# Performance work log

Hardware: AMD Instinct MI355X
Metric: run time of the kernel (lower is better)

## Reference

```python
import jax, jax.numpy as jnp
import numpy as np

NB_HEAD = 16
SIZE_PER_HEAD = 64
D_MODEL = NB_HEAD * SIZE_PER_HEAD  # 1024
B, L = 2, 2048
NEG_BIG = 1e12


def setup_inputs() -> dict:
    key = jax.random.key(0)
    ks = jax.random.split(key, 8)
    return {
        "Q_seq": jax.random.normal(ks[0], (B, L, D_MODEL), dtype=jnp.float32),
        "K_seq": jax.random.normal(ks[1], (B, L, D_MODEL), dtype=jnp.float32),
        "V_seq": jax.random.normal(ks[2], (B, L, D_MODEL), dtype=jnp.float32),
        "q_len": jax.random.randint(ks[3], (B, 1), 1, L, dtype=jnp.int32),
        "v_len": jax.random.randint(ks[4], (B, 1), 1, L, dtype=jnp.int32),
        "WQ": jax.random.normal(ks[5], (D_MODEL, D_MODEL), dtype=jnp.float32) * 0.02,
        "WK": jax.random.normal(ks[6], (D_MODEL, D_MODEL), dtype=jnp.float32) * 0.02,
        "WV": jax.random.normal(ks[7], (D_MODEL, D_MODEL), dtype=jnp.float32) * 0.02,
    }


def _len_mask(lens, length, dtype):
    # Keras code: mask = 1 - cumsum(one_hot(len, L)) -> 1 for pos < len, 0 otherwise
    return (jnp.arange(length)[None, :] < lens).astype(dtype)  # [B, L]


def reference(Q_seq, K_seq, V_seq, q_len, v_len, WQ, WK, WV):
    Bq, Lq, _ = Q_seq.shape
    Lk = K_seq.shape[1]
    # QKV projections, split heads: [B, H, L, D]
    q = (Q_seq @ WQ).reshape(Bq, Lq, NB_HEAD, SIZE_PER_HEAD).transpose(0, 2, 1, 3)
    k = (K_seq @ WK).reshape(Bq, Lk, NB_HEAD, SIZE_PER_HEAD).transpose(0, 2, 1, 3)
    v = (V_seq @ WV).reshape(Bq, Lk, NB_HEAD, SIZE_PER_HEAD).transpose(0, 2, 1, 3)
    # scaled dot-product scores [B, H, Lq, Lk]
    scores = jnp.einsum("bhqd,bhkd->bhqk", q, k) / np.float32(SIZE_PER_HEAD ** 0.5)
    # additive key-length mask (V_len), matching Mask(..., 'add')
    kmask = _len_mask(v_len, Lk, scores.dtype)  # [B, Lk]
    scores = scores - (1.0 - kmask)[:, None, None, :] * np.float32(NEG_BIG)
    A = jax.nn.softmax(scores, axis=-1)
    # attention output, merge heads: [B, Lq, H*D]
    O = jnp.einsum("bhqk,bhkd->bqhd", A, v).reshape(Bq, Lq, D_MODEL)
    # multiplicative query-length mask (Q_len), matching Mask(..., 'mul')
    qmask = _len_mask(q_len, Lq, O.dtype)  # [B, Lq]
    return O * qmask[:, :, None]
```

## Files before the change

kernel.cpp:

```cpp
#include <hip/hip_runtime.h>
#include <cstddef>

#define NB_HEAD 16
#define HEAD_DIM 64
#define D_MODEL 1024
#define BATCH 2
#define SEQ 2048
#define MROWS (BATCH * SEQ)
#define NSPLIT 3

typedef __bf16 bf16x8 __attribute__((ext_vector_type(8)));
typedef __bf16 bf16x4 __attribute__((ext_vector_type(4)));
typedef __bf16 bf16x2 __attribute__((ext_vector_type(2)));
typedef float  f32x4  __attribute__((ext_vector_type(4)));

#define XEL ((size_t)MROWS * D_MODEL)
#define WEL ((size_t)D_MODEL * D_MODEL)

#define QSCALE 0.18033688011112042f

static __device__ __forceinline__ size_t xchunk(int row, int k) {
    return ((size_t)(row >> 4) * 32 + (k >> 5)) * 512 + ((k >> 3) & 3) * 128 + (row & 15) * 8 + (k & 7);
}
static __device__ __forceinline__ size_t qkbase(int bh, int row16, int dc) {
    return ((size_t)(bh * 128 + row16) * 2 + dc) * 512;
}
static __device__ __forceinline__ size_t qkelem(int bh, int row, int d) {
    return qkbase(bh, row >> 4, d >> 5) + ((d >> 3) & 3) * 128 + (row & 15) * 8 + (d & 7);
}
static __device__ __forceinline__ size_t vbase(int bh, int d16, int kc) {
    return ((size_t)(bh * 4 + d16) * 64 + kc) * 512;
}
static __device__ __forceinline__ size_t velem(int bh, int d, int key) {
    return vbase(bh, d >> 4, key >> 5) + ((key >> 3) & 3) * 128 + (d & 15) * 8 + (key & 7);
}

static __device__ __forceinline__ void split_bf16(float x, __bf16& h, __bf16& l) {
    h = (__bf16)x;
    l = (__bf16)(x - (float)h);
}

static __device__ __forceinline__ void gload_lds16(const __bf16* g, __bf16* l) {
    __builtin_amdgcn_global_load_lds((const __attribute__((address_space(1))) void*)g,
                                     (__attribute__((address_space(3))) void*)l,
                                     16, 0, 0);
}

__global__ __launch_bounds__(256) void conv_wt_kernel(
    const float* __restrict__ W0, const float* __restrict__ W1,
    const float* __restrict__ W2,
    __bf16* __restrict__ hi, __bf16* __restrict__ lo)
{
    __shared__ float tile[64][65];
    const int t  = threadIdx.x;
    const int k0 = blockIdx.x * 64;
    const int n0 = blockIdx.y * 64;
    const int z  = blockIdx.z;
    const float* W = (z == 0) ? W0 : ((z == 1) ? W1 : W2);
    __bf16* hz = hi + (size_t)z * WEL;
    __bf16* lz = lo + (size_t)z * WEL;

    #pragma unroll
    for (int p = 0; p < 4; ++p) {
        const int e = (p * 256 + t) * 4;
        const int r = e >> 6, c = e & 63;
        const float4 v = *(const float4*)(W + (size_t)(k0 + r) * D_MODEL + n0 + c);
        tile[r][c] = v.x; tile[r][c + 1] = v.y; tile[r][c + 2] = v.z; tile[r][c + 3] = v.w;
    }
    __syncthreads();
    #pragma unroll
    for (int p = 0; p < 4; ++p) {
        const int e = (p * 256 + t) * 4;
        const int n = e >> 6, kc = e & 63;
        __bf16 h[4], l[4];
        #pragma unroll
        for (int u = 0; u < 4; ++u) split_bf16(tile[kc + u][n], h[u], l[u]);
        const size_t a = xchunk(n0 + n, k0 + kc);
        *(bf16x4*)(hz + a) = (bf16x4){h[0], h[1], h[2], h[3]};
        *(bf16x4*)(lz + a) = (bf16x4){l[0], l[1], l[2], l[3]};
    }
}

__global__ __launch_bounds__(256) void conv_x_kernel(
    const float* __restrict__ X0, const float* __restrict__ X1,
    const float* __restrict__ X2,
    const int* __restrict__ q_len, const int* __restrict__ v_len,
    __bf16* __restrict__ xhi, __bf16* __restrict__ xlo)
{
    const int z = blockIdx.y;
    const size_t e = ((size_t)blockIdx.x * 256 + threadIdx.x) * 8;
    const int l = (int)(e >> 10), k = (int)(e & 1023);
    const int bb = l >> 11, lb = l & (SEQ - 1);
    const int len = (z == 0) ? q_len[bb] : v_len[bb];
    if (lb >= ((len + 127) & ~127)) return;

    const float* X = (z == 0) ? X0 : ((z == 1) ? X1 : X2);
    const float4 v0 = *(const float4*)(X + e);
    const float4 v1 = *(const float4*)(X + e + 4);
    const float xs[8] = {v0.x, v0.y, v0.z, v0.w, v1.x, v1.y, v1.z, v1.w};
    bf16x8 h8, l8;
    #pragma unroll
    for (int u = 0; u < 8; ++u) { __bf16 h_, l_; split_bf16(xs[u], h_, l_); h8[u] = h_; l8[u] = l_; }
    const size_t a = z * XEL + xchunk(l, k);
    *(bf16x8*)(xhi + a) = h8;
    *(bf16x8*)(xlo + a) = l8;
}

__global__ __launch_bounds__(256, 3) void proj_mfma_kernel(
    const __bf16* __restrict__ Xhi, const __bf16* __restrict__ Xlo,
    const __bf16* __restrict__ Wchi, const __bf16* __restrict__ Wclo,
    const int* __restrict__ q_len, const int* __restrict__ v_len,
    __bf16* __restrict__ qch, __bf16* __restrict__ qcl,
    __bf16* __restrict__ kch, __bf16* __restrict__ kcl,
    __bf16* __restrict__ vch, __bf16* __restrict__ vcl)
{
    __shared__ __align__(16) __bf16 lds[2][16][512];

    const int t    = threadIdx.x;
    const int wave = t >> 6, lane = t & 63;
    const int li   = lane & 15, grp = lane >> 4;
    const int wm   = wave >> 1, wn = wave & 1;
    const int m0   = blockIdx.x * 128;
    const int n0   = blockIdx.y * 64;
    const int z    = blockIdx.z;
    const int bb   = m0 >> 11;
    const int l0   = m0 & (SEQ - 1);
    const int need = (z == 0) ? q_len[bb] : v_len[bb];
    if (l0 >= need) return;

    const __bf16* Xh = Xhi + z * XEL;
    const __bf16* Xl = Xlo + z * XEL;
    const __bf16* Wh = Wchi + z * WEL;
    const __bf16* Wl = Wclo + z * WEL;

    const __bf16* gsA[4];
    #pragma unroll
    for (int u = 0; u < 4; ++u) {
        const int c = u * 4 + wave;
        const __bf16* src = (c < 8) ? Xh : Xl;
        const int idx = (m0 >> 4) + (c & 7);
        gsA[u] = src + (size_t)idx * 32 * 512 + (size_t)lane * 8;
    }

    const __bf16* gBh[2];
    const __bf16* gBl[2];
    #pragma unroll
    for (int j = 0; j < 2; ++j) {
        const int idx = (n0 >> 4) + wn * 2 + j;
        gBh[j] = Wh + (size_t)idx * 32 * 512 + (size_t)lane * 8;
        gBl[j] = Wl + (size_t)idx * 32 * 512 + (size_t)lane * 8;
    }

    auto STAGE = [&](int buf, int kc) {
        #pragma unroll
        for (int u = 0; u < 4; ++u)
            gload_lds16(gsA[u] + (size_t)kc * 512, &lds[buf][u * 4 + wave][0]);
    };

    f32x4 acc[4][2] = {};
    bf16x8 bhc[2], blc[2], bhn[2], bln[2];

    STAGE(0, 0);
    #pragma unroll
    for (int j = 0; j < 2; ++j) {
        bhc[j] = *(const bf16x8*)(gBh[j]);
        blc[j] = *(const bf16x8*)(gBl[j]);
    }
    __syncthreads();

    #pragma unroll 2
    for (int kc = 0; kc < 32; ++kc) {
        const int cur = kc & 1;
        if (kc < 31) {
            STAGE(cur ^ 1, kc + 1);
            #pragma unroll
            for (int j = 0; j < 2; ++j) {
                bhn[j] = *(const bf16x8*)(gBh[j] + (size_t)(kc + 1) * 512);
                bln[j] = *(const bf16x8*)(gBl[j] + (size_t)(kc + 1) * 512);
            }
        }

        bf16x8 ah[4], al4[4];
        #pragma unroll
        for (int i = 0; i < 4; ++i) {
            ah[i]  = *(const bf16x8*)&lds[cur][(wm << 2) + i][lane * 8];
            al4[i] = *(const bf16x8*)&lds[cur][8 + (wm << 2) + i][lane * 8];
        }
        #pragma unroll
        for (int j = 0; j < 2; ++j) {
            #pragma unroll
            for (int i = 0; i < 4; ++i) {
                acc[i][j] = __builtin_amdgcn_mfma_f32_16x16x32_bf16(ah[i],  bhc[j], acc[i][j], 0, 0, 0);
                acc[i][j] = __builtin_amdgcn_mfma_f32_16x16x32_bf16(ah[i],  blc[j], acc[i][j], 0, 0, 0);
                acc[i][j] = __builtin_amdgcn_mfma_f32_16x16x32_bf16(al4[i], bhc[j], acc[i][j], 0, 0, 0);
            }
        }
        __syncthreads();
        #pragma unroll
        for (int j = 0; j < 2; ++j) { bhc[j] = bhn[j]; blc[j] = bln[j]; }
    }

    #pragma unroll
    for (int j = 0; j < 2; ++j) {
        const int cg = n0 + wn * 32 + j * 16 + li;
        const int hd = cg >> 6, d = cg & 63;
        const int bhI = bb * NB_HEAD + hd;
        #pragma unroll
        for (int i = 0; i < 4; ++i) {
            #pragma unroll
            for (int r = 0; r < 4; ++r) {
                const int rg = m0 + wm * 64 + i * 16 + grp * 4 + r;
                const int lg = rg & (SEQ - 1);
                __bf16 h_, l_;
                if (z == 0) {
                    split_bf16(acc[i][j][r] * QSCALE, h_, l_);
                    const size_t a = qkelem(bhI, lg, d);
                    qch[a] = h_; qcl[a] = l_;
                } else if (z == 1) {
                    split_bf16(acc[i][j][r], h_, l_);
                    const size_t a = qkelem(bhI, lg, d);
                    kch[a] = h_; kcl[a] = l_;
                } else {
                    split_bf16(acc[i][j][r], h_, l_);
                    const size_t a = velem(bhI, d, lg);
                    vch[a] = h_; vcl[a] = l_;
                }
            }
        }
    }
}

__global__ __launch_bounds__(256, 2) void attn_mfma_kernel(
    const __bf16* __restrict__ qch, const __bf16* __restrict__ qcl,
    const __bf16* __restrict__ kch, const __bf16* __restrict__ kcl,
    const __bf16* __restrict__ vch, const __bf16* __restrict__ vcl,
    const int* __restrict__ q_len, const int* __restrict__ v_len,
    float* __restrict__ Opart, float* __restrict__ Mbuf, float* __restrict__ Lbuf)
{
    __shared__ __align__(16) __bf16 Ps[128][72];

    const int t = threadIdx.x;
    const int wq = t >> 6, lane = t & 63;
    const int grp = lane >> 4, li = lane & 15;
    const int hh = blockIdx.x;
    const int split = (int)(blockIdx.y % NSPLIT);
    const int q0 = (int)(blockIdx.y / NSPLIT) * 128;
    const int b  = blockIdx.z;
    const int qlen = q_len[b], vlen = v_len[b];
    const int bh = b * NB_HEAD + hh;
    const int qbase = q0 + wq * 32;

    if (qbase >= qlen) return;

    bf16x8 onesv;
    #pragma unroll
    for (int u = 0; u < 8; ++u) onesv[u] = (__bf16)1.0f;

    bf16x8 qh[2][2], ql[2][2];
    #pragma unroll
    for (int s = 0; s < 2; ++s)
        #pragma unroll
        for (int ks = 0; ks < 2; ++ks) {
            const size_t a = qkbase(bh, (qbase >> 4) + s, ks) + lane * 8;
            qh[s][ks] = *(const bf16x8*)(qch + a);
            ql[s][ks] = *(const bf16x8*)(qcl + a);
        }

    f32x4 O[2][4] = {};
    float m_s[2] = {-1e30f, -1e30f};
    float l_s[2][4];
    #pragma unroll
    for (int s = 0; s < 2; ++s)
        #pragma unroll
        for (int r = 0; r < 4; ++r) l_s[s][r] = 0.f;

    const int nktT = (vlen + 63) >> 6;
    const int part = (nktT + NSPLIT - 1) / NSPLIT;
    const int tBeg = split * part;
    const int tEnd = (nktT < tBeg + part) ? nktT : (tBeg + part);

    for (int tt = tBeg; tt < tEnd; ++tt) {
        const int k0 = tt * 64;
        const bool full = (k0 + 64 <= vlen);

        f32x4 sacc[2][4] = {};
        #pragma unroll
        for (int ks = 0; ks < 2; ++ks) {
            bf16x8 kh_[4], kl_[4];
            #pragma unroll
            for (int j = 0; j < 4; ++j) {
                const size_t a = qkbase(bh, (k0 >> 4) + j, ks) + lane * 8;
                kh_[j] = *(const bf16x8*)(kch + a);
                kl_[j] = *(const bf16x8*)(kcl + a);
            }
            __builtin_amdgcn_s_setprio(1);
            #pragma unroll
            for (int j = 0; j < 4; ++j)
                #pragma unroll
                for (int s = 0; s < 2; ++s) {
                    sacc[s][j] = __builtin_amdgcn_mfma_f32_16x16x32_bf16(kh_[j], qh[s][ks], sacc[s][j], 0, 0, 0);
                    sacc[s][j] = __builtin_amdgcn_mfma_f32_16x16x32_bf16(kl_[j], qh[s][ks], sacc[s][j], 0, 0, 0);
                    sacc[s][j] = __builtin_amdgcn_mfma_f32_16x16x32_bf16(kh_[j], ql[s][ks], sacc[s][j], 0, 0, 0);
                }
            __builtin_amdgcn_s_setprio(0);
        }

        bf16x8 vh_[2][4], vl_[2][4];
        #pragma unroll
        for (int ks = 0; ks < 2; ++ks)
            #pragma unroll
            for (int j = 0; j < 4; ++j) {
                const size_t a = vbase(bh, j, (k0 >> 5) + ks) + lane * 8;
                vh_[ks][j] = *(const bf16x8*)(vch + a);
                vl_[ks][j] = *(const bf16x8*)(vcl + a);
            }

        float mx[2];
        int defer = 1;
        #pragma unroll
        for (int s = 0; s < 2; ++s) {
            if (!full) {
                #pragma unroll
                for (int j = 0; j < 4; ++j) {
                    const int keyb = k0 + j * 16 + grp * 4;
                    #pragma unroll
                    for (int r = 0; r < 4; ++r)
                        if (keyb + r >= vlen) sacc[s][j][r] = -1e30f;
                }
            }
            float m0_ = -1e30f;
            #pragma unroll
            for (int j = 0; j < 4; ++j)
                #pragma unroll
                for (int r = 0; r < 4; ++r) m0_ = fmaxf(m0_, sacc[s][j][r]);
            m0_ = fmaxf(m0_, __shfl_xor(m0_, 16));
            m0_ = fmaxf(m0_, __shfl_xor(m0_, 32));
            mx[s] = m0_;
            defer &= (m0_ - m_s[s] <= 8.f) ? 1 : 0;
        }

        if (!__all(defer)) {
            #pragma unroll
            for (int s = 0; s < 2; ++s) {
                const float mn = fmaxf(m_s[s], mx[s]);
                const float alq = exp2f(m_s[s] - mn);
                m_s[s] = mn;
                #pragma unroll
                for (int r = 0; r < 4; ++r) {
                    const float alr = __shfl(alq, grp * 4 + r);
                    l_s[s][r] *= alr;
                    #pragma unroll
                    for (int j = 0; j < 4; ++j) O[s][j][r] *= alr;
                }
            }
        }

        #pragma unroll
        for (int s = 0; s < 2; ++s) {
            const int row = wq * 32 + s * 16 + li;
            #pragma unroll
            for (int j = 0; j < 4; ++j) {
                const int col = j * 16 + grp * 4;
                bf16x2 w01, w23;
                w01[0] = (__bf16)exp2f(sacc[s][j][0] - m_s[s]);
                w01[1] = (__bf16)exp2f(sacc[s][j][1] - m_s[s]);
                w23[0] = (__bf16)exp2f(sacc[s][j][2] - m_s[s]);
                w23[1] = (__bf16)exp2f(sacc[s][j][3] - m_s[s]);
                *(bf16x2*)&Ps[row][col]     = w01;
                *(bf16x2*)&Ps[row][col + 2] = w23;
            }
        }
        asm volatile("s_waitcnt lgkmcnt(0)" ::: "memory");

        bf16x8 pa[2][2];
        #pragma unroll
        for (int s = 0; s < 2; ++s)
            #pragma unroll
            for (int ks = 0; ks < 2; ++ks)
                pa[s][ks] = *(const bf16x8*)&Ps[wq * 32 + s * 16 + li][ks * 32 + grp * 8];

        __builtin_amdgcn_s_setprio(1);
        #pragma unroll
        for (int s = 0; s < 2; ++s) {
            f32x4 lsum = {};
            lsum = __builtin_amdgcn_mfma_f32_16x16x32_bf16(pa[s][0], onesv, lsum, 0, 0, 0);
            lsum = __builtin_amdgcn_mfma_f32_16x16x32_bf16(pa[s][1], onesv, lsum, 0, 0, 0);
            #pragma unroll
            for (int r = 0; r < 4; ++r) l_s[s][r] += lsum[r];
        }

        #pragma unroll
        for (int ks = 0; ks < 2; ++ks)
            #pragma unroll
            for (int j = 0; j < 4; ++j)
                #pragma unroll
                for (int s = 0; s < 2; ++s) {
                    O[s][j] = __builtin_amdgcn_mfma_f32_16x16x32_bf16(pa[s][ks], vh_[ks][j], O[s][j], 0, 0, 0);
                    O[s][j] = __builtin_amdgcn_mfma_f32_16x16x32_bf16(pa[s][ks], vl_[ks][j], O[s][j], 0, 0, 0);
                }
        __builtin_amdgcn_s_setprio(0);
    }

    const size_t osplit = (size_t)split * MROWS * D_MODEL;
    #pragma unroll
    for (int s = 0; s < 2; ++s)
        #pragma unroll
        for (int r = 0; r < 4; ++r) {
            const int q = qbase + s * 16 + grp * 4 + r;
            if (q < qlen) {
                #pragma unroll
                for (int j = 0; j < 4; ++j)
                    Opart[osplit + ((size_t)b * SEQ + q) * D_MODEL + hh * HEAD_DIM + j * 16 + li] = O[s][j][r];
                if (li == 0) {
                    const size_t mi = (((size_t)split * BATCH + b) * NB_HEAD + hh) * SEQ + q;
                    Lbuf[mi] = l_s[s][r];
                }
            }
        }
    #pragma unroll
    for (int s = 0; s < 2; ++s) {
        const int q = qbase + s * 16 + li;
        if (grp == 0 && q < qlen) {
            const size_t mi = (((size_t)split * BATCH + b) * NB_HEAD + hh) * SEQ + q;
            Mbuf[mi] = m_s[s];
        }
    }
}

__global__ __launch_bounds__(256) void attn_merge_kernel(
    const float* __restrict__ Opart, const float* __restrict__ Mbuf,
    const float* __restrict__ Lbuf, const int* __restrict__ q_len,
    float* __restrict__ out)
{
    const int row = blockIdx.x;
    const int b = row >> 11, q = row & (SEQ - 1);
    const int col = threadIdx.x * 4;
    const int hh = col >> 6;
    const size_t oidx = (size_t)row * D_MODEL + col;

    float4 o = make_float4(0.f, 0.f, 0.f, 0.f);
    if (q < q_len[b]) {
        const size_t mlsz = (size_t)BATCH * NB_HEAD * SEQ;
        const size_t mi = ((size_t)b * NB_HEAD + hh) * SEQ + q;
        float ms[NSPLIT], ls[NSPLIT];
        float M = -1e30f;
        #pragma unroll
        for (int s = 0; s < NSPLIT; ++s) {
            ms[s] = Mbuf[s * mlsz + mi];
            ls[s] = Lbuf[s * mlsz + mi];
            M = fmaxf(M, ms[s]);
        }
        float denom = 0.f;
        float w[NSPLIT];
        #pragma unroll
        for (int s = 0; s < NSPLIT; ++s) {
            w[s] = exp2f(ms[s] - M);
            denom += ls[s] * w[s];
        }
        const float inv = 1.f / denom;
        float acc[4] = {0.f, 0.f, 0.f, 0.f};
        #pragma unroll
        for (int s = 0; s < NSPLIT; ++s) {
            const float4 a = *(const float4*)(Opart + (size_t)s * MROWS * D_MODEL + oidx);
            acc[0] += a.x * w[s]; acc[1] += a.y * w[s];
            acc[2] += a.z * w[s]; acc[3] += a.w * w[s];
        }
        o.x = acc[0] * inv; o.y = acc[1] * inv; o.z = acc[2] * inv; o.w = acc[3] * inv;
    }
    *(float4*)(out + oidx) = o;
}

extern "C" void kernel_launch(void* const* d_in, const int* in_sizes, int n_in,
                              void* d_out, int out_size, void* d_ws, size_t ws_size,
                              hipStream_t stream)
{
    (void)in_sizes; (void)n_in; (void)out_size; (void)ws_size;
    const float* Q_seq = (const float*)d_in[0];
    const float* K_seq = (const float*)d_in[1];
    const float* V_seq = (const float*)d_in[2];
    const int*   q_len = (const int*)d_in[3];
    const int*   v_len = (const int*)d_in[4];
    const float* WQ    = (const float*)d_in[5];
    const float* WK    = (const float*)d_in[6];
    const float* WV    = (const float*)d_in[7];
    float* out = (float*)d_out;

    __bf16* wchi = (__bf16*)d_ws;
    __bf16* wclo = wchi + 3 * WEL;
    __bf16* xhi_ = wclo + 3 * WEL;
    __bf16* xlo_ = xhi_ + 3 * XEL;
    __bf16* qch_ = xlo_ + 3 * XEL;
    __bf16* qcl_ = qch_ + XEL;
    __bf16* kch_ = qcl_ + XEL;
    __bf16* kcl_ = kch_ + XEL;
    __bf16* vch_ = kcl_ + XEL;
    __bf16* vcl_ = vch_ + XEL;

    float* Opart = (float*)xhi_;
    float* Mbuf  = (float*)wchi;
    float* Lbuf  = Mbuf + (size_t)NSPLIT * BATCH * NB_HEAD * SEQ;

    dim3 blk(256);

    dim3 cg(D_MODEL / 64, D_MODEL / 64, 3);
    conv_wt_kernel<<<cg, blk, 0, stream>>>(WQ, WK, WV, wchi, wclo);

    dim3 xg((unsigned)(XEL / 2048), 3);
    conv_x_kernel<<<xg, blk, 0, stream>>>(Q_seq, K_seq, V_seq, q_len, v_len, xhi_, xlo_);

    dim3 pg(MROWS / 128, D_MODEL / 64, 3);
    proj_mfma_kernel<<<pg, blk, 0, stream>>>(xhi_, xlo_, wchi, wclo, q_len, v_len,
                                             qch_, qcl_, kch_, kcl_, vch_, vcl_);

    dim3 ag(NB_HEAD, (SEQ / 128) * NSPLIT, BATCH);
    attn_mfma_kernel<<<ag, blk, 0, stream>>>(qch_, qcl_, kch_, kcl_, vch_, vcl_,
                                             q_len, v_len, Opart, Mbuf, Lbuf);

    attn_merge_kernel<<<dim3(MROWS), blk, 0, stream>>>(Opart, Mbuf, Lbuf, q_len, out);
}
```

Measured before the change: 255.7 us.

## Triple-buffer projection GEMM with two-stage prefetch and partial vmcnt waits

Converts the projection kernel's double-buffered K loop into a three-stage pipeline. A tiles go to LDS and B fragments go to registers, both loaded two iterations ahead. Full __syncthreads is replaced by explicit s_waitcnt vmcnt(8) plus s_barrier, so in-flight loads for the next stage overlap the MFMAs. The loop is fully unrolled with sched_barriers to pin the order, at the cost of more LDS (48KB vs 32KB) and more VGPRs, which may reduce occupancy below the 3 blocks per CU launch bound.

Measured after the change: 268.2 us. 4.9% more time.

```diff
diff --git a/kernel.cpp b/kernel.cpp
--- a/kernel.cpp
+++ b/kernel.cpp
@@ -114,7 +114,7 @@
     __bf16* __restrict__ kch, __bf16* __restrict__ kcl,
     __bf16* __restrict__ vch, __bf16* __restrict__ vcl)
 {
-    __shared__ __align__(16) __bf16 lds[2][16][512];
+    __shared__ __align__(16) __bf16 lds[3][16][512];
 
     const int t    = threadIdx.x;
     const int wave = t >> 6, lane = t & 63;
@@ -151,34 +151,37 @@
         gBl[j] = Wl + (size_t)idx * 32 * 512 + (size_t)lane * 8;
     }
 
-    auto STAGE = [&](int buf, int kc) {
+    bf16x8 bH[3][2], bL[3][2];
+
+    auto STAGE_A = [&](int buf, int kc) {
         #pragma unroll
         for (int u = 0; u < 4; ++u)
             gload_lds16(gsA[u] + (size_t)kc * 512, &lds[buf][u * 4 + wave][0]);
     };
+    auto LOAD_B = [&](int set, int kc) {
+        #pragma unroll
+        for (int j = 0; j < 2; ++j) {
+            bH[set][j] = *(const bf16x8*)(gBh[j] + (size_t)kc * 512);
+            bL[set][j] = *(const bf16x8*)(gBl[j] + (size_t)kc * 512);
+        }
+    };
 
     f32x4 acc[4][2] = {};
-    bf16x8 bhc[2], blc[2], bhn[2], bln[2];
-
-    STAGE(0, 0);
-    #pragma unroll
-    for (int j = 0; j < 2; ++j) {
-        bhc[j] = *(const bf16x8*)(gBh[j]);
-        blc[j] = *(const bf16x8*)(gBl[j]);
-    }
-    __syncthreads();
-
-    #pragma unroll 2
+
+    STAGE_A(0, 0); LOAD_B(0, 0);
+    STAGE_A(1, 1); LOAD_B(1, 1);
+    asm volatile("s_waitcnt vmcnt(8)" ::: "memory");
+    __builtin_amdgcn_s_barrier();
+    __builtin_amdgcn_sched_barrier(0);
+
+    #pragma unroll
     for (int kc = 0; kc < 32; ++kc) {
-        const int cur = kc & 1;
-        if (kc < 31) {
-            STAGE(cur ^ 1, kc + 1);
-            #pragma unroll
-            for (int j = 0; j < 2; ++j) {
-                bhn[j] = *(const bf16x8*)(gBh[j] + (size_t)(kc + 1) * 512);
-                bln[j] = *(const bf16x8*)(gBl[j] + (size_t)(kc + 1) * 512);
-            }
-        }
+        const int cur = kc % 3;
+        if (kc + 2 < 32) {
+            STAGE_A((kc + 2) % 3, kc + 2);
+            LOAD_B((kc + 2) % 3, kc + 2);
+        }
+        __builtin_amdgcn_sched_barrier(0);
 
         bf16x8 ah[4], al4[4];
         #pragma unroll
@@ -190,14 +193,21 @@
         for (int j = 0; j < 2; ++j) {
             #pragma unroll
             for (int i = 0; i < 4; ++i) {
-                acc[i][j] = __builtin_amdgcn_mfma_f32_16x16x32_bf16(ah[i],  bhc[j], acc[i][j], 0, 0, 0);
-                acc[i][j] = __builtin_amdgcn_mfma_f32_16x16x32_bf16(ah[i],  blc[j], acc[i][j], 0, 0, 0);
-                acc[i][j] = __builtin_amdgcn_mfma_f32_16x16x32_bf16(al4[i], bhc[j], acc[i][j], 0, 0, 0);
-            }
-        }
-        __syncthreads();
-        #pragma unroll
-        for (int j = 0; j < 2; ++j) { bhc[j] = bhn[j]; blc[j] = bln[j]; }
+                acc[i][j] = __builtin_amdgcn_mfma_f32_16x16x32_bf16(ah[i],  bH[cur][j], acc[i][j], 0, 0, 0);
+                acc[i][j] = __builtin_amdgcn_mfma_f32_16x16x32_bf16(ah[i],  bL[cur][j], acc[i][j], 0, 0, 0);
+                acc[i][j] = __builtin_amdgcn_mfma_f32_16x16x32_bf16(al4[i], bH[cur][j], acc[i][j], 0, 0, 0);
+            }
+        }
+
+        if (kc < 30) {
+            asm volatile("s_waitcnt vmcnt(8)" ::: "memory");
+            __builtin_amdgcn_s_barrier();
+            __builtin_amdgcn_sched_barrier(0);
+        } else if (kc == 30) {
+            asm volatile("s_waitcnt vmcnt(0)" ::: "memory");
+            __builtin_amdgcn_s_barrier();
+            __builtin_amdgcn_sched_barrier(0);
+        }
     }
 
     #pragma unroll
```
